# Optimization experiments

Hardware: AMD Instinct MI355X
Metric: run time of the kernel (lower is better)

## Reference

```python
import jax, jax.numpy as jnp
import numpy as np

D_MODEL = 1024
N_HEADS = 16
CHUNK_LEN = 50
MEM_LEN = 16
TOTAL_PROB = 20000
TOTAL_SKILL = 1000
B = 64
L = 2000
EPS = 1e-5


def _layernorm(x, g, b):
    mu = jnp.mean(x, axis=-1, keepdims=True)
    var = jnp.var(x, axis=-1, keepdims=True)
    return (x - mu) * jax.lax.rsqrt(var + EPS) * g + b


def setup_inputs() -> dict:
    key = jax.random.key(0)
    ks = jax.random.split(key, 20)
    s = 0.02
    D = D_MODEL
    emb_problem = (jax.random.normal(ks[0], (TOTAL_PROB, D), jnp.float32) * s).at[0].set(0.0)  # padding_idx=0
    emb_skill = (jax.random.normal(ks[1], (TOTAL_SKILL, D), jnp.float32) * s).at[0].set(0.0)
    mem_init = jax.random.normal(ks[2], (1, MEM_LEN, D), jnp.float32) * s
    pos_emb = jax.random.normal(ks[3], (MEM_LEN + CHUNK_LEN, D), jnp.float32) * s
    w_qkv = jax.random.normal(ks[4], (3 * D, D), jnp.float32) * s
    b_qkv = jnp.zeros((3 * D,), jnp.float32)
    w_out = jax.random.normal(ks[5], (D, D), jnp.float32) * s
    b_out = jnp.zeros((D,), jnp.float32)
    w1 = jax.random.normal(ks[6], (4 * D, D), jnp.float32) * s
    b1 = jnp.zeros((4 * D,), jnp.float32)
    w2 = jax.random.normal(ks[7], (D, 4 * D), jnp.float32) * s
    b2 = jnp.zeros((D,), jnp.float32)
    g_attn = jnp.ones((D,), jnp.float32)
    be_attn = jnp.zeros((D,), jnp.float32)
    g_ffn = jnp.ones((D,), jnp.float32)
    be_ffn = jnp.zeros((D,), jnp.float32)
    w_gate = jax.random.normal(ks[8], (D, D), jnp.float32) * s
    b_gate = jnp.zeros((D,), jnp.float32)
    in_prob = jax.random.randint(ks[9], (B, L), 0, TOTAL_PROB, dtype=jnp.int64 if jax.config.jax_enable_x64 else jnp.int32)
    in_skill = jax.random.randint(ks[10], (B, L), 0, TOTAL_SKILL, dtype=jnp.int64 if jax.config.jax_enable_x64 else jnp.int32)
    return dict(in_prob=in_prob, in_skill=in_skill, emb_problem=emb_problem, emb_skill=emb_skill,
                mem_init=mem_init, pos_emb=pos_emb, w_qkv=w_qkv, b_qkv=b_qkv, w_out=w_out, b_out=b_out,
                w1=w1, b1=b1, w2=w2, b2=b2, g_attn=g_attn, be_attn=be_attn, g_ffn=g_ffn, be_ffn=be_ffn,
                w_gate=w_gate, b_gate=b_gate)


def _mha(z, w_qkv, b_qkv, w_out, b_out, mask):
    # z: [B, T, D]; mask: [T, T] bool, True = disallowed (torch attn_mask semantics)
    Bz, T, D = z.shape
    dh = D // N_HEADS
    qkv = z @ w_qkv.T + b_qkv  # [B, T, 3D]
    q, k, v = jnp.split(qkv, 3, axis=-1)
    def heads(x):
        return x.reshape(Bz, T, N_HEADS, dh).transpose(0, 2, 1, 3)  # [B, H, T, dh]
    q, k, v = heads(q), heads(k), heads(v)
    scores = jnp.einsum('bhqd,bhkd->bhqk', q, k) / jnp.sqrt(jnp.float32(dh))
    scores = jnp.where(mask[None, None], jnp.float32(-1e9), scores)
    a = jax.nn.softmax(scores, axis=-1)
    o = jnp.einsum('bhqk,bhkd->bhqd', a, v)  # [B, H, T, dh]
    o = o.transpose(0, 2, 1, 3).reshape(Bz, T, D)
    return o @ w_out.T + b_out


def reference(in_prob, in_skill, emb_problem, emb_skill, mem_init, pos_emb,
              w_qkv, b_qkv, w_out, b_out, w1, b1, w2, b2,
              g_attn, be_attn, g_ffn, be_ffn, w_gate, b_gate):
    Bx, Lx = in_prob.shape
    D = emb_problem.shape[1]
    x = emb_problem[in_prob] + emb_skill[in_skill]  # [B, L, D]
    n_chunks = Lx // CHUNK_LEN
    T = MEM_LEN + CHUNK_LEN
    # block mask: memory fully visible, chunk part strictly causal
    causal = jnp.triu(jnp.ones((CHUNK_LEN, CHUNK_LEN), bool), k=1)
    mask = jnp.zeros((T, T), bool).at[MEM_LEN:, MEM_LEN:].set(causal)
    pos = pos_emb[:T][None]  # [1, T, D]
    chunks = x.reshape(Bx, n_chunks, CHUNK_LEN, D).transpose(1, 0, 2, 3)  # [K, B, Lc, D]
    mem0 = jnp.broadcast_to(mem_init, (Bx, MEM_LEN, D))

    def step(mem, xs):
        chunk, kidx = xs
        z = jnp.concatenate([mem, chunk], axis=1) + pos  # [B, T, D]
        z = z + _mha(_layernorm(z, g_attn, be_attn), w_qkv, b_qkv, w_out, b_out, mask)
        h = _layernorm(z, g_ffn, be_ffn)
        z = z + (jax.nn.relu(h @ w1.T + b1) @ w2.T + b2)
        mem_cand = z[:, :MEM_LEN]
        h_k = z[:, MEM_LEN:]
        g = jax.nn.sigmoid(mem_cand @ w_gate.T + b_gate)
        mem_gated = g * mem_cand + (1.0 - g) * mem
        mem_new = jnp.where(kidx == 0, mem_cand, mem_gated)  # first chunk: no gate
        return mem_new, h_k

    mem_final, hs = jax.lax.scan(step, mem0, (chunks, jnp.arange(n_chunks)))
    enc_out = hs.transpose(1, 0, 2, 3).reshape(Bx, Lx, D)
    return enc_out, mem_final
```

## Files before the change

### kernel.cpp

```cpp
#include <hip/hip_runtime.h>
#include <hip/hip_bf16.h>

#define D_MODEL 1024
#define N_HEADS 16
#define DH 64
#define CHUNK_LEN 50
#define MEM_LEN 16
#define TT 66
#define BB 64
#define LL 2000
#define NCHUNK 40
#define MTOK (BB*TT)

typedef _Float16 half8_t __attribute__((ext_vector_type(8)));
typedef __attribute__((ext_vector_type(4))) float f32x4;

typedef __attribute__((address_space(1))) const void GVoid;
typedef __attribute__((address_space(3))) void LVoid;

__device__ __forceinline__ void gload16(const void* g, void* l) {
  __builtin_amdgcn_global_load_lds((GVoid*)g, (LVoid*)l, 16, 0, 0);
}

__global__ __launch_bounds__(256) void f2h_kernel(const float* __restrict__ in,
                                                  _Float16* __restrict__ out, int n) {
  int i = (blockIdx.x * 256 + threadIdx.x) * 4;
  if (i < n) {
    float4 v = *(const float4*)(in + i);
    out[i+0] = (_Float16)v.x;
    out[i+1] = (_Float16)v.y;
    out[i+2] = (_Float16)v.z;
    out[i+3] = (_Float16)v.w;
  }
}

__global__ __launch_bounds__(256) void build_z_ln(
    const int* __restrict__ in_prob, const int* __restrict__ in_skill,
    const float* __restrict__ emb_p, const float* __restrict__ emb_s,
    const float* __restrict__ mem_src, int mem_bstride,
    const float* __restrict__ pos,
    const float* __restrict__ gam, const float* __restrict__ bet,
    float* __restrict__ z, _Float16* __restrict__ zn, int chunk)
{
  int row = blockIdx.x;
  int b = row / TT, t = row % TT;
  int tid = threadIdx.x;
  int d = tid * 4;
  float4 v;
  if (t < MEM_LEN) {
    v = *(const float4*)(mem_src + (size_t)b*mem_bstride + t*D_MODEL + d);
  } else {
    int tok = chunk*CHUNK_LEN + (t - MEM_LEN);
    int p = in_prob[b*LL + tok];
    int s = in_skill[b*LL + tok];
    float4 vp = *(const float4*)(emb_p + (size_t)p*D_MODEL + d);
    float4 vs = *(const float4*)(emb_s + (size_t)s*D_MODEL + d);
    v = make_float4(vp.x+vs.x, vp.y+vs.y, vp.z+vs.z, vp.w+vs.w);
  }
  float4 pv = *(const float4*)(pos + t*D_MODEL + d);
  v.x += pv.x; v.y += pv.y; v.z += pv.z; v.w += pv.w;
  *(float4*)(z + (size_t)row*D_MODEL + d) = v;
  float sum = v.x+v.y+v.z+v.w;
  float sq  = v.x*v.x+v.y*v.y+v.z*v.z+v.w*v.w;
  #pragma unroll
  for (int off = 32; off; off >>= 1) {
    sum += __shfl_down(sum, off, 64);
    sq  += __shfl_down(sq,  off, 64);
  }
  __shared__ float rs_[4], rq_[4];
  int wave = tid >> 6, lane = tid & 63;
  if (lane == 0) { rs_[wave] = sum; rq_[wave] = sq; }
  __syncthreads();
  sum = rs_[0]+rs_[1]+rs_[2]+rs_[3];
  sq  = rq_[0]+rq_[1]+rq_[2]+rq_[3];
  float mu  = sum * (1.0f/D_MODEL);
  float var = sq  * (1.0f/D_MODEL) - mu*mu;
  float rstd = rsqrtf(var + 1e-5f);
  float4 gv = *(const float4*)(gam + d);
  float4 bv = *(const float4*)(bet + d);
  _Float16* o = zn + (size_t)row*D_MODEL + d;
  o[0] = (_Float16)((v.x-mu)*rstd*gv.x + bv.x);
  o[1] = (_Float16)((v.y-mu)*rstd*gv.y + bv.y);
  o[2] = (_Float16)((v.z-mu)*rstd*gv.z + bv.z);
  o[3] = (_Float16)((v.w-mu)*rstd*gv.w + bv.w);
}

__global__ __launch_bounds__(256) void ln_kernel(
    const float* __restrict__ z, const float* __restrict__ gam, const float* __restrict__ bet,
    _Float16* __restrict__ out)
{
  int row = blockIdx.x;
  int tid = threadIdx.x;
  int d = tid * 4;
  float4 v = *(const float4*)(z + (size_t)row*D_MODEL + d);
  float sum = v.x+v.y+v.z+v.w;
  float sq  = v.x*v.x+v.y*v.y+v.z*v.z+v.w*v.w;
  #pragma unroll
  for (int off = 32; off; off >>= 1) {
    sum += __shfl_down(sum, off, 64);
    sq  += __shfl_down(sq,  off, 64);
  }
  __shared__ float rs_[4], rq_[4];
  int wave = tid >> 6, lane = tid & 63;
  if (lane == 0) { rs_[wave] = sum; rq_[wave] = sq; }
  __syncthreads();
  sum = rs_[0]+rs_[1]+rs_[2]+rs_[3];
  sq  = rq_[0]+rq_[1]+rq_[2]+rq_[3];
  float mu  = sum * (1.0f/D_MODEL);
  float var = sq  * (1.0f/D_MODEL) - mu*mu;
  float rstd = rsqrtf(var + 1e-5f);
  float4 gv = *(const float4*)(gam + d);
  float4 bv = *(const float4*)(bet + d);
  _Float16* o = out + (size_t)row*D_MODEL + d;
  o[0] = (_Float16)((v.x-mu)*rstd*gv.x + bv.x);
  o[1] = (_Float16)((v.y-mu)*rstd*gv.y + bv.y);
  o[2] = (_Float16)((v.z-mu)*rstd*gv.z + bv.z);
  o[3] = (_Float16)((v.w-mu)*rstd*gv.w + bv.w);
}

__global__ __launch_bounds__(256) void attn_kernel(
    const _Float16* __restrict__ qkv, _Float16* __restrict__ attn_o)
{
  __shared__ float qs[TT*DH];
  __shared__ float ks_t[DH*67];
  __shared__ float vs[TT*DH];
  __shared__ float sc[TT*67];
  int bh = blockIdx.x; int b = bh >> 4, h = bh & 15;
  int tid = threadIdx.x;
  const _Float16* base = qkv + (size_t)b*TT*3072 + h*DH;
  for (int i = tid; i < TT*DH; i += 256) {
    int t = i >> 6, d2 = i & 63;
    const _Float16* rp = base + (size_t)t*3072 + d2;
    qs[i] = (float)rp[0];
    ks_t[d2*67 + t] = (float)rp[1024];
    vs[i] = (float)rp[2048];
  }
  __syncthreads();
  for (int p = tid; p < TT*TT; p += 256) {
    int qi = p / TT, kj = p % TT;
    float s;
    if (qi >= MEM_LEN && kj >= MEM_LEN && kj > qi) {
      s = -1e9f;
    } else {
      float acc = 0.f;
      const float* qr = qs + qi*DH;
      #pragma unroll 8
      for (int d2 = 0; d2 < DH; d2++) acc += qr[d2]*ks_t[d2*67 + kj];
      s = acc * 0.125f;
    }
    sc[qi*67 + kj] = s;
  }
  __syncthreads();
  if (tid < TT) {
    float* r = sc + tid*67;
    float m = -1e30f;
    for (int j = 0; j < TT; j++) m = fmaxf(m, r[j]);
    float ssum = 0.f;
    for (int j = 0; j < TT; j++) { float e = __expf(r[j]-m); r[j] = e; ssum += e; }
    float inv = 1.f/ssum;
    for (int j = 0; j < TT; j++) r[j] *= inv;
  }
  __syncthreads();
  for (int p = tid; p < TT*DH; p += 256) {
    int qi = p >> 6, d2 = p & 63;
    float acc = 0.f;
    const float* ar = sc + qi*67;
    for (int kj = 0; kj < TT; kj++) acc += ar[kj]*vs[kj*DH + d2];
    attn_o[((size_t)b*TT + qi)*D_MODEL + h*DH + d2] = (_Float16)acc;
  }
}

__global__ __launch_bounds__(256) void finalize_reduce(
    const float* __restrict__ z, const float* __restrict__ p0, const float* __restrict__ p1,
    const float* __restrict__ b2,
    float* __restrict__ enc_out, float* __restrict__ mem,
    _Float16* __restrict__ mcb, float* __restrict__ mcf, int chunk)
{
  int row = blockIdx.x; int b = row / TT, t = row % TT;
  int d = threadIdx.x * 4;
  size_t idx = (size_t)row*D_MODEL + d;
  float4 v  = *(const float4*)(z  + idx);
  float4 a0 = *(const float4*)(p0 + idx);
  float4 a1 = *(const float4*)(p1 + idx);
  float4 bv = *(const float4*)(b2 + d);
  v.x += a0.x + a1.x + bv.x;
  v.y += a0.y + a1.y + bv.y;
  v.z += a0.z + a1.z + bv.z;
  v.w += a0.w + a1.w + bv.w;
  if (t >= MEM_LEN) {
    size_t o = ((size_t)b*LL + chunk*CHUNK_LEN + (t - MEM_LEN))*D_MODEL + d;
    *(float4*)(enc_out + o) = v;
  } else {
    size_t mrow = (size_t)b*MEM_LEN + t;
    if (chunk == 0) {
      *(float4*)(mem + mrow*D_MODEL + d) = v;
    } else {
      *(float4*)(mcf + mrow*D_MODEL + d) = v;
      _Float16* o = mcb + mrow*D_MODEL + d;
      o[0] = (_Float16)v.x;
      o[1] = (_Float16)v.y;
      o[2] = (_Float16)v.z;
      o[3] = (_Float16)v.w;
    }
  }
}

__global__ __launch_bounds__(256) void copy_mem_kernel(const float* __restrict__ mem,
                                                       float* __restrict__ out) {
  int i = (blockIdx.x * 256 + threadIdx.x) * 4;
  float4 v = *(const float4*)(mem + i);
  *(float4*)(out + i) = v;
}

#define EPI_QKV   0
#define EPI_RESID 1
#define EPI_RELU  2
#define EPI_PART  3

#define KSLICE 2048

template<int EPI>
__global__ __launch_bounds__(256) void gemm_bt(
    const _Float16* __restrict__ A,
    const _Float16* __restrict__ Bw,
    const float* __restrict__ bias,
    float* __restrict__ zres,
    _Float16* __restrict__ obf,
    float* __restrict__ p1,
    int K, int lda, int ldo)
{
  __shared__ short As[128*32];
  __shared__ short Bs[128*32];
  int tid = threadIdx.x;
  int lane = tid & 63, wave = tid >> 6;
  int wr = wave >> 1, wc = wave & 1;
  int tm = blockIdx.y * 128, tn = blockIdx.x * 128;
  f32x4 acc[4][4] = {};
  const short* Ash = (const short*)A;
  const short* Bsh = (const short*)Bw;
  if constexpr (EPI == EPI_PART) {
    Ash += (size_t)blockIdx.z * KSLICE;
    Bsh += (size_t)blockIdx.z * KSLICE;
  }
  int e0 = tid * 8;
  int r0 = e0 >> 5, c0 = e0 & 31;

  for (int kt = 0; kt < K; kt += 32) {
    gload16(Ash + (size_t)(tm +      r0)*lda + kt + c0, (char*)As +        wave*1024);
    gload16(Ash + (size_t)(tm + 64 + r0)*lda + kt + c0, (char*)As + 4096 + wave*1024);
    gload16(Bsh + (size_t)(tn +      r0)*lda + kt + c0, (char*)Bs +        wave*1024);
    gload16(Bsh + (size_t)(tn + 64 + r0)*lda + kt + c0, (char*)Bs + 4096 + wave*1024);
    __syncthreads();
    half8_t af[4], bfr[4];
    int ko = (lane >> 4) * 8;
    int rr = lane & 15;
    #pragma unroll
    for (int m = 0; m < 4; m++)
      af[m] = *(const half8_t*)(As + (wr*64 + m*16 + rr)*32 + ko);
    #pragma unroll
    for (int n = 0; n < 4; n++)
      bfr[n] = *(const half8_t*)(Bs + (wc*64 + n*16 + rr)*32 + ko);
    #pragma unroll
    for (int m = 0; m < 4; m++)
      #pragma unroll
      for (int n = 0; n < 4; n++)
        acc[m][n] = __builtin_amdgcn_mfma_f32_16x16x32_f16(af[m], bfr[n], acc[m][n], 0, 0, 0);
    __syncthreads();
  }

  int rbase = tm + wr*64 + ((lane >> 4) << 2);
  int cbase = tn + wc*64 + (lane & 15);
  float* pp = nullptr;
  if constexpr (EPI == EPI_PART) pp = (blockIdx.z == 0) ? zres : p1;
  #pragma unroll
  for (int n = 0; n < 4; n++) {
    int col = cbase + n*16;
    float bs = (EPI == EPI_PART) ? 0.f : bias[col];
    #pragma unroll
    for (int m = 0; m < 4; m++) {
      #pragma unroll
      for (int i = 0; i < 4; i++) {
        int r = rbase + m*16 + i;
        float v = acc[m][n][i] + bs;
        if constexpr (EPI == EPI_QKV) {
          obf[(size_t)r*ldo + col] = (_Float16)v;
        } else if constexpr (EPI == EPI_RESID) {
          zres[(size_t)r*D_MODEL + col] += v;
        } else if constexpr (EPI == EPI_RELU) {
          obf[(size_t)r*ldo + col] = (_Float16)fmaxf(v, 0.f);
        } else {
          pp[(size_t)r*D_MODEL + col] = v;
        }
      }
    }
  }
}

__global__ __launch_bounds__(256) void gemm_gate64(
    const _Float16* __restrict__ A,
    const _Float16* __restrict__ Bw,
    const float* __restrict__ bias,
    const float* __restrict__ mcf,
    float* __restrict__ mem)
{
  __shared__ short As[64*32];
  __shared__ short Bs[64*32];
  int tid = threadIdx.x;
  int lane = tid & 63, wave = tid >> 6;
  int wr = wave >> 1, wc = wave & 1;
  int tm = blockIdx.y * 64, tn = blockIdx.x * 64;
  f32x4 acc[2][2] = {};
  const short* Ash = (const short*)A;
  const short* Bsh = (const short*)Bw;
  int e0 = tid * 8;
  int r0 = e0 >> 5, c0 = e0 & 31;

  for (int kt = 0; kt < 1024; kt += 32) {
    gload16(Ash + (size_t)(tm + r0)*1024 + kt + c0, (char*)As + wave*1024);
    gload16(Bsh + (size_t)(tn + r0)*1024 + kt + c0, (char*)Bs + wave*1024);
    __syncthreads();
    half8_t af[2], bfr[2];
    int ko = (lane >> 4) * 8;
    int rr = lane & 15;
    #pragma unroll
    for (int m = 0; m < 2; m++)
      af[m] = *(const half8_t*)(As + (wr*32 + m*16 + rr)*32 + ko);
    #pragma unroll
    for (int n = 0; n < 2; n++)
      bfr[n] = *(const half8_t*)(Bs + (wc*32 + n*16 + rr)*32 + ko);
    #pragma unroll
    for (int m = 0; m < 2; m++)
      #pragma unroll
      for (int n = 0; n < 2; n++)
        acc[m][n] = __builtin_amdgcn_mfma_f32_16x16x32_f16(af[m], bfr[n], acc[m][n], 0, 0, 0);
    __syncthreads();
  }

  int rbase = tm + wr*32 + ((lane >> 4) << 2);
  int cbase = tn + wc*32 + (lane & 15);
  #pragma unroll
  for (int n = 0; n < 2; n++) {
    int col = cbase + n*16;
    float bs = bias[col];
    #pragma unroll
    for (int m = 0; m < 2; m++) {
      #pragma unroll
      for (int i = 0; i < 4; i++) {
        int r = rbase + m*16 + i;
        float g = 1.f / (1.f + __expf(-(acc[m][n][i] + bs)));
        size_t mi = (size_t)r*D_MODEL + col;
        mem[mi] = g*mcf[mi] + (1.f - g)*mem[mi];
      }
    }
  }
}

extern "C" void kernel_launch(void* const* d_in, const int* in_sizes, int n_in,
                              void* d_out, int out_size, void* d_ws, size_t ws_size,
                              hipStream_t stream) {
  const int*   in_prob  = (const int*)d_in[0];
  const int*   in_skill = (const int*)d_in[1];
  const float* emb_p    = (const float*)d_in[2];
  const float* emb_s    = (const float*)d_in[3];
  const float* mem_init = (const float*)d_in[4];
  const float* pos      = (const float*)d_in[5];
  const float* w_qkv    = (const float*)d_in[6];
  const float* b_qkv    = (const float*)d_in[7];
  const float* w_out    = (const float*)d_in[8];
  const float* b_out    = (const float*)d_in[9];
  const float* w1       = (const float*)d_in[10];
  const float* b1       = (const float*)d_in[11];
  const float* w2       = (const float*)d_in[12];
  const float* b2       = (const float*)d_in[13];
  const float* g_attn   = (const float*)d_in[14];
  const float* be_attn  = (const float*)d_in[15];
  const float* g_ffn    = (const float*)d_in[16];
  const float* be_ffn   = (const float*)d_in[17];
  const float* w_gate   = (const float*)d_in[18];
  const float* b_gate   = (const float*)d_in[19];

  float* enc_out = (float*)d_out;
  float* mem_out = enc_out + (size_t)BB*LL*D_MODEL;

  char* ws = (char*)d_ws;
  size_t off = 0;
  auto alloc = [&](size_t bytes) -> char* {
    char* p = ws + off;
    off += (bytes + 255) & ~(size_t)255;
    return p;
  };
  _Float16* wqkv_h = (_Float16*)alloc((size_t)3072*1024*2);
  _Float16* wout_h = (_Float16*)alloc((size_t)1024*1024*2);
  _Float16* w1_h   = (_Float16*)alloc((size_t)4096*1024*2);
  _Float16* w2_h   = (_Float16*)alloc((size_t)1024*4096*2);
  _Float16* wgate_h= (_Float16*)alloc((size_t)1024*1024*2);
  float*    z      = (float*)alloc((size_t)MTOK*D_MODEL*4);
  _Float16* zn     = (_Float16*)alloc((size_t)MTOK*D_MODEL*2);
  _Float16* qkv    = (_Float16*)alloc((size_t)MTOK*3072*2);
  _Float16* ao     = (_Float16*)alloc((size_t)MTOK*D_MODEL*2);
  _Float16* hb     = (_Float16*)alloc((size_t)MTOK*D_MODEL*2);
  _Float16* fh     = (_Float16*)alloc((size_t)MTOK*4096*2);
  _Float16* mcb    = (_Float16*)alloc((size_t)1024*1024*2);
  float*    mem    = (float*)alloc((size_t)1024*1024*4);
  float*    mcf    = (float*)alloc((size_t)1024*1024*4);
  float*    part0  = (float*)alloc((size_t)MTOK*D_MODEL*4);
  float*    part1  = (float*)alloc((size_t)MTOK*D_MODEL*4);
  if (off > ws_size) return;

  f2h_kernel<<<(3072*1024)/1024, 256, 0, stream>>>(w_qkv, wqkv_h, 3072*1024);
  f2h_kernel<<<(1024*1024)/1024, 256, 0, stream>>>(w_out, wout_h, 1024*1024);
  f2h_kernel<<<(4096*1024)/1024, 256, 0, stream>>>(w1, w1_h, 4096*1024);
  f2h_kernel<<<(1024*4096)/1024, 256, 0, stream>>>(w2, w2_h, 1024*4096);
  f2h_kernel<<<(1024*1024)/1024, 256, 0, stream>>>(w_gate, wgate_h, 1024*1024);

  for (int c = 0; c < NCHUNK; c++) {
    const float* msrc = (c == 0) ? mem_init : mem;
    int mbs = (c == 0) ? 0 : MEM_LEN*D_MODEL;
    build_z_ln<<<MTOK, 256, 0, stream>>>(in_prob, in_skill, emb_p, emb_s,
                                         msrc, mbs, pos, g_attn, be_attn, z, zn, c);
    gemm_bt<EPI_QKV><<<dim3(3072/128, MTOK/128), 256, 0, stream>>>(
        zn, wqkv_h, b_qkv, nullptr, qkv, nullptr, 1024, 1024, 3072);
    attn_kernel<<<BB*N_HEADS, 256, 0, stream>>>(qkv, ao);
    gemm_bt<EPI_RESID><<<dim3(1024/128, MTOK/128), 256, 0, stream>>>(
        ao, wout_h, b_out, z, nullptr, nullptr, 1024, 1024, 1024);
    ln_kernel<<<MTOK, 256, 0, stream>>>(z, g_ffn, be_ffn, hb);
    gemm_bt<EPI_RELU><<<dim3(4096/128, MTOK/128), 256, 0, stream>>>(
        hb, w1_h, b1, nullptr, fh, nullptr, 1024, 1024, 4096);
    gemm_bt<EPI_PART><<<dim3(1024/128, MTOK/128, 2), 256, 0, stream>>>(
        fh, w2_h, b2, part0, nullptr, part1, KSLICE, 4096, 1024);
    finalize_reduce<<<MTOK, 256, 0, stream>>>(z, part0, part1, b2,
                                              enc_out, mem, mcb, mcf, c);
    if (c > 0) {
      gemm_gate64<<<dim3(1024/64, 1024/64), 256, 0, stream>>>(
          mcb, wgate_h, b_gate, mcf, mem);
    }
  }
  copy_mem_kernel<<<(1024*1024)/1024, 256, 0, stream>>>(mem, mem_out);
}
```

Before: 12.95 ms.

## Double-buffer GEMM LDS staging and register-tile the attention matmuls

```diff
diff --git a/kernel.cpp b/kernel.cpp
--- a/kernel.cpp
+++ b/kernel.cpp
@@ -121,8 +121,8 @@
 __global__ __launch_bounds__(256) void attn_kernel(
     const _Float16* __restrict__ qkv, _Float16* __restrict__ attn_o)
 {
-  __shared__ float qs[TT*DH];
-  __shared__ float ks_t[DH*67];
+  __shared__ float qs_t[64*68 + 8];
+  __shared__ float ks_t[64*68 + 8];
   __shared__ float vs[TT*DH];
   __shared__ float sc[TT*67];
   int bh = blockIdx.x; int b = bh >> 4, h = bh & 15;
@@ -131,24 +131,45 @@
   for (int i = tid; i < TT*DH; i += 256) {
     int t = i >> 6, d2 = i & 63;
     const _Float16* rp = base + (size_t)t*3072 + d2;
-    qs[i] = (float)rp[0];
-    ks_t[d2*67 + t] = (float)rp[1024];
-    vs[i] = (float)rp[2048];
-  }
-  __syncthreads();
-  for (int p = tid; p < TT*TT; p += 256) {
-    int qi = p / TT, kj = p % TT;
-    float s;
-    if (qi >= MEM_LEN && kj >= MEM_LEN && kj > qi) {
-      s = -1e9f;
-    } else {
-      float acc = 0.f;
-      const float* qr = qs + qi*DH;
-      #pragma unroll 8
-      for (int d2 = 0; d2 < DH; d2++) acc += qr[d2]*ks_t[d2*67 + kj];
-      s = acc * 0.125f;
-    }
-    sc[qi*67 + kj] = s;
+    qs_t[d2*68 + t] = (float)rp[0];
+    ks_t[d2*68 + t] = (float)rp[1024];
+    vs[t*64 + d2]   = (float)rp[2048];
+  }
+  __syncthreads();
+  if (tid < 153) {
+    int ti = tid / 9, tj = tid % 9;
+    int qi0 = ti*4, kj0 = tj*8;
+    float acc[4][8];
+    #pragma unroll
+    for (int i = 0; i < 4; i++)
+      #pragma unroll
+      for (int j = 0; j < 8; j++) acc[i][j] = 0.f;
+    for (int d2 = 0; d2 < 64; d2++) {
+      float4 qv = *(const float4*)(qs_t + d2*68 + qi0);
+      float4 k0 = *(const float4*)(ks_t + d2*68 + kj0);
+      float4 k1 = *(const float4*)(ks_t + d2*68 + kj0 + 4);
+      float q_[4] = {qv.x, qv.y, qv.z, qv.w};
+      float k_[8] = {k0.x, k0.y, k0.z, k0.w, k1.x, k1.y, k1.z, k1.w};
+      #pragma unroll
+      for (int i = 0; i < 4; i++)
+        #pragma unroll
+        for (int j = 0; j < 8; j++)
+          acc[i][j] += q_[i]*k_[j];
+    }
+    #pragma unroll
+    for (int i = 0; i < 4; i++) {
+      int qi = qi0 + i;
+      if (qi >= TT) continue;
+      #pragma unroll
+      for (int j = 0; j < 8; j++) {
+        int kj = kj0 + j;
+        if (kj >= TT) continue;
+        float s;
+        if (qi >= MEM_LEN && kj >= MEM_LEN && kj > qi) s = -1e9f;
+        else s = acc[i][j]*0.125f;
+        sc[qi*67 + kj] = s;
+      }
+    }
   }
   __syncthreads();
   if (tid < TT) {
@@ -161,12 +182,36 @@
     for (int j = 0; j < TT; j++) r[j] *= inv;
   }
   __syncthreads();
-  for (int p = tid; p < TT*DH; p += 256) {
-    int qi = p >> 6, d2 = p & 63;
-    float acc = 0.f;
-    const float* ar = sc + qi*67;
-    for (int kj = 0; kj < TT; kj++) acc += ar[kj]*vs[kj*DH + d2];
-    attn_o[((size_t)b*TT + qi)*D_MODEL + h*DH + d2] = (_Float16)acc;
+  if (tid < 136) {
+    int ti = tid >> 3, tj = tid & 7;
+    int qi0 = ti*4, d20 = tj*8;
+    float acc[4][8];
+    #pragma unroll
+    for (int i = 0; i < 4; i++)
+      #pragma unroll
+      for (int j = 0; j < 8; j++) acc[i][j] = 0.f;
+    for (int kj = 0; kj < TT; kj++) {
+      float a_[4];
+      #pragma unroll
+      for (int i = 0; i < 4; i++)
+        a_[i] = (qi0 + i < TT) ? sc[(qi0+i)*67 + kj] : 0.f;
+      float4 v0 = *(const float4*)(vs + kj*64 + d20);
+      float4 v1 = *(const float4*)(vs + kj*64 + d20 + 4);
+      float v_[8] = {v0.x, v0.y, v0.z, v0.w, v1.x, v1.y, v1.z, v1.w};
+      #pragma unroll
+      for (int i = 0; i < 4; i++)
+        #pragma unroll
+        for (int j = 0; j < 8; j++)
+          acc[i][j] += a_[i]*v_[j];
+    }
+    #pragma unroll
+    for (int i = 0; i < 4; i++) {
+      int qi = qi0 + i;
+      if (qi >= TT) continue;
+      _Float16* o = attn_o + ((size_t)b*TT + qi)*D_MODEL + h*DH + d20;
+      #pragma unroll
+      for (int j = 0; j < 8; j++) o[j] = (_Float16)acc[i][j];
+    }
   }
 }
 
@@ -229,8 +274,8 @@
     float* __restrict__ p1,
     int K, int lda, int ldo)
 {
-  __shared__ short As[128*32];
-  __shared__ short Bs[128*32];
+  __shared__ short As[2][128*32];
+  __shared__ short Bs[2][128*32];
   int tid = threadIdx.x;
   int lane = tid & 63, wave = tid >> 6;
   int wr = wave >> 1, wc = wave & 1;
@@ -244,29 +289,40 @@
   }
   int e0 = tid * 8;
   int r0 = e0 >> 5, c0 = e0 & 31;
-
-  for (int kt = 0; kt < K; kt += 32) {
-    gload16(Ash + (size_t)(tm +      r0)*lda + kt + c0, (char*)As +        wave*1024);
-    gload16(Ash + (size_t)(tm + 64 + r0)*lda + kt + c0, (char*)As + 4096 + wave*1024);
-    gload16(Bsh + (size_t)(tn +      r0)*lda + kt + c0, (char*)Bs +        wave*1024);
-    gload16(Bsh + (size_t)(tn + 64 + r0)*lda + kt + c0, (char*)Bs + 4096 + wave*1024);
-    __syncthreads();
+  int ko = (lane >> 4) * 8;
+  int rr = lane & 15;
+
+  auto STAGE = [&](int buf, int kt) {
+    gload16(Ash + (size_t)(tm +      r0)*lda + kt + c0, (char*)&As[buf][0] +        wave*1024);
+    gload16(Ash + (size_t)(tm + 64 + r0)*lda + kt + c0, (char*)&As[buf][0] + 4096 + wave*1024);
+    gload16(Bsh + (size_t)(tn +      r0)*lda + kt + c0, (char*)&Bs[buf][0] +        wave*1024);
+    gload16(Bsh + (size_t)(tn + 64 + r0)*lda + kt + c0, (char*)&Bs[buf][0] + 4096 + wave*1024);
+  };
+  auto COMPUTE = [&](int buf) {
     half8_t af[4], bfr[4];
-    int ko = (lane >> 4) * 8;
-    int rr = lane & 15;
     #pragma unroll
     for (int m = 0; m < 4; m++)
-      af[m] = *(const half8_t*)(As + (wr*64 + m*16 + rr)*32 + ko);
+      af[m] = *(const half8_t*)(&As[buf][(wr*64 + m*16 + rr)*32 + ko]);
     #pragma unroll
     for (int n = 0; n < 4; n++)
-      bfr[n] = *(const half8_t*)(Bs + (wc*64 + n*16 + rr)*32 + ko);
+      bfr[n] = *(const half8_t*)(&Bs[buf][(wc*64 + n*16 + rr)*32 + ko]);
     #pragma unroll
     for (int m = 0; m < 4; m++)
       #pragma unroll
       for (int n = 0; n < 4; n++)
         acc[m][n] = __builtin_amdgcn_mfma_f32_16x16x32_f16(af[m], bfr[n], acc[m][n], 0, 0, 0);
+  };
+
+  STAGE(0, 0);
+  __syncthreads();
+  int cur = 0;
+  for (int kt = 32; kt < K; kt += 32) {
+    STAGE(cur ^ 1, kt);
+    COMPUTE(cur);
     __syncthreads();
-  }
+    cur ^= 1;
+  }
+  COMPUTE(cur);
 
   int rbase = tm + wr*64 + ((lane >> 4) << 2);
   int cbase = tn + wc*64 + (lane & 15);
```

Result: faster. 11.98 ms (-7.5%).
